# Performance work log

Measured on AMD Instinct MI355X. Metric: run time of the kernel, lower is better.

Reference implementation:

```python
import jax, jax.numpy as jnp
import numpy as np

B, T, DM, DQ, DA, F, K = 128, 1024, 512, 1024, 128, 32, 31


def setup_inputs() -> dict:
    key = jax.random.key(0)
    ks = jax.random.split(key, 9)
    state = jax.random.uniform(ks[1], (B, T), dtype=jnp.float32)
    state = state / jnp.sum(state, axis=-1, keepdims=True)  # alignment-like
    return {
        "query": jax.random.normal(ks[0], (B, DQ), dtype=jnp.float32),
        "state": state,
        "prev_max_alignments": jax.random.randint(ks[2], (B,), 0, T, dtype=jnp.int32),
        "memory": jax.random.normal(ks[3], (B, T, DM), dtype=jnp.float32),
        "Wq": jax.random.normal(ks[4], (DQ, DA), dtype=jnp.float32) * 0.02,
        "Wmem": jax.random.normal(ks[5], (DM, DA), dtype=jnp.float32) * 0.02,
        "conv_k": jax.random.normal(ks[6], (K, 1, F), dtype=jnp.float32) * 0.02,
        "Wloc": jax.random.normal(ks[7], (F, DA), dtype=jnp.float32) * 0.02,
        "v_w": jax.random.normal(ks[8], (DA,), dtype=jnp.float32) * 0.02,
        "v_b": jnp.zeros((), dtype=jnp.float32),
    }


def reference(query, state, prev_max_alignments, memory, Wq, Wmem, conv_k, Wloc, v_w, v_b):
    # processed query: [B, 1, DA]
    pq = (query @ Wq)[:, None, :]
    # location features: Conv1D 'same', no bias, over cumulative alignments [B, T, 1]
    f = jax.lax.conv_general_dilated(
        state[:, :, None], conv_k,
        window_strides=(1,), padding="SAME",
        dimension_numbers=("NWC", "WIO", "NWC"),
    )  # [B, T, F]
    loc = f @ Wloc                      # [B, T, DA]
    keys = memory @ Wmem                # [B, T, DA]
    # additive tanh score -> [B, T]
    energy = jnp.tanh(keys + pq + loc) @ v_w + v_b
    alignments = jax.nn.softmax(energy, axis=-1)
    new_state = alignments + state      # is_cumulate=True
    # context: [B, DM]
    context = jnp.einsum("bt,btd->bd", alignments, memory)
    return context, alignments, new_state
```

## Files before the change

### kernel.cpp

```cpp
#include <hip/hip_runtime.h>
#include <math.h>

#define B  128
#define T  1024
#define DM 512
#define DQ 1024
#define DA 128
#define F  32
#define KW 31

typedef short s16x8 __attribute__((ext_vector_type(8)));
typedef float f32x4 __attribute__((ext_vector_type(4)));
typedef unsigned int u32;
typedef u32 u32x4 __attribute__((ext_vector_type(4)));
typedef __attribute__((address_space(1))) const unsigned int gu32;
typedef __attribute__((address_space(3))) unsigned int lu32;

__device__ __forceinline__ unsigned short f2bf(float f) {
    u32 u = __builtin_bit_cast(u32, f);
    u32 r = u + 0x7FFFu + ((u >> 16) & 1u);
    return (unsigned short)(r >> 16);
}
__device__ __forceinline__ float bf2f(unsigned short h) {
    u32 u = ((u32)h) << 16;
    return __builtin_bit_cast(float, u);
}
__device__ __forceinline__ float fast_tanh(float x) {
    float ax = fabsf(x);
    float e = __expf(-2.0f * ax);
    float t = 1.0f - 2.0f * e / (1.0f + e);
    return copysignf(t, x);
}

__device__ __forceinline__ void trunc_split_pack(f32x4 a, f32x4 b, s16x8& hi, s16x8& lo) {
    u32x4 hw, lw;
    #pragma unroll
    for (int p = 0; p < 4; ++p) {
        float f0 = (p < 2) ? a[2 * p] : b[2 * p - 4];
        float f1 = (p < 2) ? a[2 * p + 1] : b[2 * p - 3];
        u32 u0 = __builtin_bit_cast(u32, f0);
        u32 u1 = __builtin_bit_cast(u32, f1);
        u32 t0 = u0 & 0xFFFF0000u;
        u32 t1 = u1 & 0xFFFF0000u;
        float l0 = f0 - __builtin_bit_cast(float, t0);
        float l1 = f1 - __builtin_bit_cast(float, t1);
        hw[p] = (u0 >> 16) | t1;
        lw[p] = (__builtin_bit_cast(u32, l0) >> 16) | (__builtin_bit_cast(u32, l1) & 0xFFFF0000u);
    }
    hi = __builtin_bit_cast(s16x8, hw);
    lo = __builtin_bit_cast(s16x8, lw);
}

__global__ __launch_bounds__(128) void prep_kernel(
        const float* __restrict__ query, const float* __restrict__ Wq,
        const float* __restrict__ Wmem, const float* __restrict__ conv_k,
        const float* __restrict__ Wloc,
        float* __restrict__ pqp, unsigned short* __restrict__ wsplit,
        unsigned short* __restrict__ CWt) {
    int a = threadIdx.x;
    int blk = blockIdx.x;
    if (blk < 4 * B) {
        int b = blk >> 2, q = blk & 3;
        const float* qp = query + b * DQ + q * 256;
        const float* wp = Wq + (size_t)(q * 256) * DA + a;
        float s = 0.f;
        #pragma unroll 4
        for (int i = 0; i < 256; ++i) s += qp[i] * wp[(size_t)i * DA];
        pqp[(q * B + b) * DA + a] = s;
    } else if (blk < 4 * B + DM) {
        int k = blk - 4 * B;
        unsigned short hi = f2bf(Wmem[k * DA + a]);
        int c = k >> 6;
        int es = (k & 63) ^ ((a & 7) << 3);
        wsplit[c * 8192 + a * 64 + es] = hi;
    } else {
        int k = blk - (4 * B + DM);
        float s = 0.f;
        if (k < KW) {
            #pragma unroll
            for (int f = 0; f < F; ++f) s += conv_k[k * F + f] * Wloc[f * DA + a];
        }
        CWt[a * 32 + k] = f2bf(s);
    }
}

__global__ __launch_bounds__(256, 4) void energy_mfma(
        const float* __restrict__ memory, const float* __restrict__ state,
        const float* __restrict__ pqp, const unsigned short* __restrict__ wsplit,
        const unsigned short* __restrict__ CWt, const float* __restrict__ v_w,
        const float* __restrict__ v_b, float* __restrict__ energy,
        float* __restrict__ pctx, float2* __restrict__ ms) {
    __shared__ unsigned short Wlds[8192];
    __shared__ unsigned short cwlds[4096];
    __shared__ float stl[160];
    __shared__ float pql[DA];
    __shared__ float vwl[DA];
    __shared__ float el[128];

    int tid = threadIdx.x;
    int w = tid >> 6, l = tid & 63, r = l & 15, g = l >> 4;
    int b  = blockIdx.x >> 3;
    int tile = blockIdx.x & 7;
    int t0 = tile << 7;

    for (int i = tid; i < 160; i += 256) {
        int t = t0 - 15 + i;
        stl[i] = (i < 159 && t >= 0 && t < T) ? state[b * T + t] : 0.f;
    }
    if (tid < DA) {
        float s = 0.f;
        #pragma unroll
        for (int q = 0; q < 4; ++q) s += pqp[(q * B + b) * DA + tid];
        pql[tid] = s;
        vwl[tid] = v_w[tid];
    }

    #pragma unroll
    for (int rd = 0; rd < 2; ++rd)
        __builtin_amdgcn_global_load_lds((gu32*)(CWt + rd * 2048 + tid * 8),
                                         (lu32*)(cwlds + (w << 9) + rd * 2048), 16, 0, 0);

    f32x4 acc0[8], acc1[8];
    #pragma unroll
    for (int nt = 0; nt < 8; ++nt) {
        acc0[nt] = (f32x4){0.f, 0.f, 0.f, 0.f};
        acc1[nt] = (f32x4){0.f, 0.f, 0.f, 0.f};
    }

    const int swz8 = (r & 7) << 3;
    const size_t arow = ((size_t)(b * T + t0 + w * 32 + r)) * DM;

    for (int c = 0; c < 8; ++c) {
        __syncthreads();
        {
            const unsigned short* src = wsplit + (size_t)c * 8192 + tid * 8;
            #pragma unroll
            for (int rd = 0; rd < 4; ++rd)
                __builtin_amdgcn_global_load_lds((gu32*)(src + rd * 2048),
                                                 (lu32*)(Wlds + (w << 9) + rd * 2048),
                                                 16, 0, 0);
        }
        __syncthreads();

        const float* Ab = memory + arow + c * 64;
        #pragma unroll
        for (int kk = 0; kk < 2; ++kk) {
            const float* p0 = Ab + kk * 32 + g * 8;
            f32x4 f00 = *(const f32x4*)p0;
            f32x4 f01 = *(const f32x4*)(p0 + 4);
            const float* p1 = p0 + 16 * DM;
            f32x4 f10 = *(const f32x4*)p1;
            f32x4 f11 = *(const f32x4*)(p1 + 4);
            s16x8 Ah0, Al0, Ah1, Al1;
            trunc_split_pack(f00, f01, Ah0, Al0);
            trunc_split_pack(f10, f11, Ah1, Al1);
            int off = (kk * 32 + g * 8) ^ swz8;
            #pragma unroll
            for (int nt = 0; nt < 8; ++nt) {
                const unsigned short* bp = Wlds + (nt * 16 + r) * 64 + off;
                s16x8 Bh = *(const s16x8*)bp;
                acc0[nt] = __builtin_amdgcn_mfma_f32_16x16x32_bf16(Ah0, Bh, acc0[nt], 0, 0, 0);
                acc0[nt] = __builtin_amdgcn_mfma_f32_16x16x32_bf16(Al0, Bh, acc0[nt], 0, 0, 0);
                acc1[nt] = __builtin_amdgcn_mfma_f32_16x16x32_bf16(Ah1, Bh, acc1[nt], 0, 0, 0);
                acc1[nt] = __builtin_amdgcn_mfma_f32_16x16x32_bf16(Al1, Bh, acc1[nt], 0, 0, 0);
            }
        }
    }

    s16x8 st0, st1;
    {
        int base0 = w * 32 + r + g * 8;
        #pragma unroll
        for (int j = 0; j < 8; ++j) {
            st0[j] = (short)f2bf(stl[base0 + j]);
            st1[j] = (short)f2bf(stl[base0 + 16 + j]);
        }
    }
    #pragma unroll
    for (int nt = 0; nt < 8; ++nt) {
        const unsigned short* cp = cwlds + (nt * 16 + r) * 32 + g * 8;
        s16x8 cw = *(const s16x8*)cp;
        acc0[nt] = __builtin_amdgcn_mfma_f32_16x16x32_bf16(st0, cw, acc0[nt], 0, 0, 0);
        acc1[nt] = __builtin_amdgcn_mfma_f32_16x16x32_bf16(st1, cw, acc1[nt], 0, 0, 0);
    }

    float vb = *v_b;
    #pragma unroll
    for (int sub = 0; sub < 2; ++sub) {
        #pragma unroll
        for (int reg = 0; reg < 4; ++reg) {
            float p = 0.f;
            #pragma unroll
            for (int nt = 0; nt < 8; ++nt) {
                int col = nt * 16 + r;
                float v = (sub == 0) ? acc0[nt][reg] : acc1[nt][reg];
                p += fast_tanh(v + pql[col]) * vwl[col];
            }
            p += __shfl_xor(p, 1, 16);
            p += __shfl_xor(p, 2, 16);
            p += __shfl_xor(p, 4, 16);
            p += __shfl_xor(p, 8, 16);
            if (r == 0) {
                int tl = w * 32 + sub * 16 + g * 4 + reg;
                energy[b * T + t0 + tl] = p + vb;
                el[tl] = p + vb;
            }
        }
    }
    __syncthreads();

    float m_w = -1e30f;
    #pragma unroll
    for (int t = 0; t < 32; ++t) m_w = fmaxf(m_w, el[w * 32 + t]);
    float s_w = 0.f;
    f32x4 c0 = (f32x4){0.f, 0.f, 0.f, 0.f};
    f32x4 c1 = (f32x4){0.f, 0.f, 0.f, 0.f};
    const float* mb = memory + ((size_t)(b * T + t0 + w * 32)) * DM + l * 8;
    #pragma unroll 4
    for (int t = 0; t < 32; ++t) {
        float pw = __expf(el[w * 32 + t] - m_w);
        s_w += pw;
        f32x4 v0 = *(const f32x4*)(mb + (size_t)t * DM);
        f32x4 v1 = *(const f32x4*)(mb + (size_t)t * DM + 4);
        c0 += pw * v0;
        c1 += pw * v1;
    }
    float* po = pctx + ((size_t)(tile * 4 + w) * B + b) * DM + l * 8;
    *(f32x4*)po = c0;
    *(f32x4*)(po + 4) = c1;
    if (l == 0) ms[(tile * 4 + w) * B + b] = make_float2(m_w, s_w);
}

__global__ __launch_bounds__(256) void finalize_kernel(
        const float* __restrict__ energy, const float* __restrict__ state,
        const float2* __restrict__ ms, const float* __restrict__ pctx,
        float* __restrict__ alignments, float* __restrict__ new_state,
        float* __restrict__ context) {
    int b = blockIdx.x, tid = threadIdx.x;
    float m = -1e30f;
    #pragma unroll
    for (int i = 0; i < 32; ++i) m = fmaxf(m, ms[i * B + b].x);
    float sc[32];
    float S = 0.f;
    #pragma unroll
    for (int i = 0; i < 32; ++i) {
        float2 v = ms[i * B + b];
        float e = __expf(v.x - m);
        sc[i] = e;
        S += e * v.y;
    }
    float invS = 1.0f / S;

    f32x4 ev = ((const f32x4*)(energy + b * T))[tid];
    f32x4 a4;
    a4[0] = __expf(ev[0] - m) * invS;
    a4[1] = __expf(ev[1] - m) * invS;
    a4[2] = __expf(ev[2] - m) * invS;
    a4[3] = __expf(ev[3] - m) * invS;
    ((f32x4*)(alignments + b * T))[tid] = a4;
    f32x4 st4 = ((const f32x4*)(state + b * T))[tid];
    ((f32x4*)(new_state + b * T))[tid] = a4 + st4;

    #pragma unroll
    for (int j = 0; j < 2; ++j) {
        int d = tid + j * 256;
        float c = 0.f;
        #pragma unroll 8
        for (int i = 0; i < 32; ++i)
            c += sc[i] * pctx[((size_t)i * B + b) * DM + d];
        context[b * DM + d] = c * invS;
    }
}

extern "C" void kernel_launch(void* const* d_in, const int* in_sizes, int n_in,
                              void* d_out, int out_size, void* d_ws, size_t ws_size,
                              hipStream_t stream) {
    const float* query  = (const float*)d_in[0];
    const float* state  = (const float*)d_in[1];
    const float* memory = (const float*)d_in[3];
    const float* Wq     = (const float*)d_in[4];
    const float* Wmem   = (const float*)d_in[5];
    const float* conv_k = (const float*)d_in[6];
    const float* Wloc   = (const float*)d_in[7];
    const float* v_w    = (const float*)d_in[8];
    const float* v_b    = (const float*)d_in[9];

    float* out        = (float*)d_out;
    float* context    = out;
    float* alignments = out + B * DM;
    float* new_state  = out + B * DM + B * T;

    char* ws = (char*)d_ws;
    float*          pqp     = (float*)ws;
    unsigned short* wsplit  = (unsigned short*)(ws + 262144);
    unsigned short* CWt     = (unsigned short*)(ws + 524288);
    float*          energy  = (float*)(ws + 532480);
    float*          pctx    = (float*)(ws + 1056768);
    float2*         ms      = (float2*)(ws + 1056768 + 8388608);

    prep_kernel<<<dim3(4 * B + DM + 32), 128, 0, stream>>>(query, Wq, Wmem, conv_k, Wloc, pqp, wsplit, CWt);
    energy_mfma<<<dim3(B * (T / 128)), 256, 0, stream>>>(memory, state, pqp, wsplit, CWt, v_w, v_b, energy, pctx, ms);
    finalize_kernel<<<dim3(B), 256, 0, stream>>>(energy, state, ms, pctx, alignments, new_state, context);
}
```

Baseline: 121.6 us.

## Prefetch memory tiles into registers and split query projection finer

The energy kernel now loads the next 64-column chunk of memory into registers while the current chunk is split into bf16 hi/lo parts and fed to MFMAs. This hides global load latency behind the matrix math. To make room for the extra registers, the occupancy hint drops from 4 to 3 blocks per CU. The query projection in the prep kernel is also split into 8 partial sums instead of 4, giving more blocks with shorter loops, and the workspace offsets are moved to fit the larger partial buffer.

```diff
diff --git a/kernel.cpp b/kernel.cpp
--- a/kernel.cpp
+++ b/kernel.cpp
@@ -59,22 +59,22 @@
         unsigned short* __restrict__ CWt) {
     int a = threadIdx.x;
     int blk = blockIdx.x;
-    if (blk < 4 * B) {
-        int b = blk >> 2, q = blk & 3;
-        const float* qp = query + b * DQ + q * 256;
-        const float* wp = Wq + (size_t)(q * 256) * DA + a;
+    if (blk < 8 * B) {
+        int b = blk >> 3, q = blk & 7;
+        const float* qp = query + b * DQ + q * 128;
+        const float* wp = Wq + (size_t)(q * 128) * DA + a;
         float s = 0.f;
         #pragma unroll 4
-        for (int i = 0; i < 256; ++i) s += qp[i] * wp[(size_t)i * DA];
+        for (int i = 0; i < 128; ++i) s += qp[i] * wp[(size_t)i * DA];
         pqp[(q * B + b) * DA + a] = s;
-    } else if (blk < 4 * B + DM) {
-        int k = blk - 4 * B;
+    } else if (blk < 8 * B + DM) {
+        int k = blk - 8 * B;
         unsigned short hi = f2bf(Wmem[k * DA + a]);
         int c = k >> 6;
         int es = (k & 63) ^ ((a & 7) << 3);
         wsplit[c * 8192 + a * 64 + es] = hi;
     } else {
-        int k = blk - (4 * B + DM);
+        int k = blk - (8 * B + DM);
         float s = 0.f;
         if (k < KW) {
             #pragma unroll
@@ -84,7 +84,7 @@
     }
 }
 
-__global__ __launch_bounds__(256, 4) void energy_mfma(
+__global__ __launch_bounds__(256, 3) void energy_mfma(
         const float* __restrict__ memory, const float* __restrict__ state,
         const float* __restrict__ pqp, const unsigned short* __restrict__ wsplit,
         const unsigned short* __restrict__ CWt, const float* __restrict__ v_w,
@@ -110,7 +110,7 @@
     if (tid < DA) {
         float s = 0.f;
         #pragma unroll
-        for (int q = 0; q < 4; ++q) s += pqp[(q * B + b) * DA + tid];
+        for (int q = 0; q < 8; ++q) s += pqp[(q * B + b) * DA + tid];
         pql[tid] = s;
         vwl[tid] = v_w[tid];
     }
@@ -129,6 +129,19 @@
 
     const int swz8 = (r & 7) << 3;
     const size_t arow = ((size_t)(b * T + t0 + w * 32 + r)) * DM;
+    const float* Abase = memory + arow + g * 8;
+
+    f32x4 rA[8], rAn[8];
+    {
+        const float* p = Abase;
+        #pragma unroll
+        for (int kk = 0; kk < 2; ++kk) {
+            rA[kk * 4 + 0] = *(const f32x4*)(p + kk * 32);
+            rA[kk * 4 + 1] = *(const f32x4*)(p + kk * 32 + 4);
+            rA[kk * 4 + 2] = *(const f32x4*)(p + kk * 32 + 16 * DM);
+            rA[kk * 4 + 3] = *(const f32x4*)(p + kk * 32 + 16 * DM + 4);
+        }
+    }
 
     for (int c = 0; c < 8; ++c) {
         __syncthreads();
@@ -142,18 +155,22 @@
         }
         __syncthreads();
 
-        const float* Ab = memory + arow + c * 64;
+        if (c < 7) {
+            const float* p = Abase + (c + 1) * 64;
+            #pragma unroll
+            for (int kk = 0; kk < 2; ++kk) {
+                rAn[kk * 4 + 0] = *(const f32x4*)(p + kk * 32);
+                rAn[kk * 4 + 1] = *(const f32x4*)(p + kk * 32 + 4);
+                rAn[kk * 4 + 2] = *(const f32x4*)(p + kk * 32 + 16 * DM);
+                rAn[kk * 4 + 3] = *(const f32x4*)(p + kk * 32 + 16 * DM + 4);
+            }
+        }
+
         #pragma unroll
         for (int kk = 0; kk < 2; ++kk) {
-            const float* p0 = Ab + kk * 32 + g * 8;
-            f32x4 f00 = *(const f32x4*)p0;
-            f32x4 f01 = *(const f32x4*)(p0 + 4);
-            const float* p1 = p0 + 16 * DM;
-            f32x4 f10 = *(const f32x4*)p1;
-            f32x4 f11 = *(const f32x4*)(p1 + 4);
             s16x8 Ah0, Al0, Ah1, Al1;
-            trunc_split_pack(f00, f01, Ah0, Al0);
-            trunc_split_pack(f10, f11, Ah1, Al1);
+            trunc_split_pack(rA[kk * 4 + 0], rA[kk * 4 + 1], Ah0, Al0);
+            trunc_split_pack(rA[kk * 4 + 2], rA[kk * 4 + 3], Ah1, Al1);
             int off = (kk * 32 + g * 8) ^ swz8;
             #pragma unroll
             for (int nt = 0; nt < 8; ++nt) {
@@ -165,6 +182,8 @@
                 acc1[nt] = __builtin_amdgcn_mfma_f32_16x16x32_bf16(Al1, Bh, acc1[nt], 0, 0, 0);
             }
         }
+        #pragma unroll
+        for (int j = 0; j < 8; ++j) rA[j] = rAn[j];
     }
 
     s16x8 st0, st1;
@@ -292,13 +311,13 @@
 
     char* ws = (char*)d_ws;
     float*          pqp     = (float*)ws;
-    unsigned short* wsplit  = (unsigned short*)(ws + 262144);
-    unsigned short* CWt     = (unsigned short*)(ws + 524288);
-    float*          energy  = (float*)(ws + 532480);
-    float*          pctx    = (float*)(ws + 1056768);
-    float2*         ms      = (float2*)(ws + 1056768 + 8388608);
-
-    prep_kernel<<<dim3(4 * B + DM + 32), 128, 0, stream>>>(query, Wq, Wmem, conv_k, Wloc, pqp, wsplit, CWt);
+    unsigned short* wsplit  = (unsigned short*)(ws + 524288);
+    unsigned short* CWt     = (unsigned short*)(ws + 655360);
+    float*          energy  = (float*)(ws + 663552);
+    float*          pctx    = (float*)(ws + 1187840);
+    float2*         ms      = (float2*)(ws + 1187840 + 8388608);
+
+    prep_kernel<<<dim3(8 * B + DM + 32), 128, 0, stream>>>(query, Wq, Wmem, conv_k, Wloc, pqp, wsplit, CWt);
     energy_mfma<<<dim3(B * (T / 128)), 256, 0, stream>>>(memory, state, pqp, wsplit, CWt, v_w, v_b, energy, pctx, ms);
     finalize_kernel<<<dim3(B), 256, 0, stream>>>(energy, state, ms, pctx, alignments, new_state, context);
 }
```

Result: no change. 120.7 us (median of 2 runs) (-0.8%).
